# Kernel optimization log

Hardware: AMD Instinct MI355X
Metric: run time of the kernel (lower is better)

## Reference

```python
import jax, jax.numpy as jnp
import numpy as np

B, A, OBS, NACT, H, D = 8192, 8, 128, 32, 256, 64  # batch, n_agents, obs_shape, n_actions, rnn_hidden_dim, attn_dim
N = B * A


def setup_inputs() -> dict:
    key = jax.random.key(0)
    ks = jax.random.split(key, 12)
    s = 0.02
    return {
        "o": jax.random.normal(ks[0], (N, OBS), dtype=jnp.float32),
        "o_next": jax.random.normal(ks[1], (N, OBS), dtype=jnp.float32),
        "h": jax.random.normal(ks[2], (N, H), dtype=jnp.float32),
        "actions": jax.random.uniform(ks[3], (N, A, NACT), dtype=jnp.float32),
        "wq_w": jax.random.normal(ks[4], (D, 2 * OBS), dtype=jnp.float32) * s,
        "wq_b": jnp.zeros((D,), dtype=jnp.float32),
        "wk_w": jax.random.normal(ks[5], (D, NACT), dtype=jnp.float32) * s,
        "wk_b": jnp.zeros((D,), dtype=jnp.float32),
        "wv1_w": jax.random.normal(ks[6], (D, H + NACT), dtype=jnp.float32) * s,
        "wv1_b": jnp.zeros((D,), dtype=jnp.float32),
        "wv2_w": jax.random.normal(ks[7], (NACT, D), dtype=jnp.float32) * s,
        "wv2_b": jnp.zeros((NACT,), dtype=jnp.float32),
    }


def reference(o, o_next, h, actions, wq_w, wq_b, wk_w, wk_b, wv1_w, wv1_b, wv2_w, wv2_b):
    n, a, nact = actions.shape           # [N, A, n_actions]
    d = wq_w.shape[0]                    # attn_dim
    hdim = h.shape[-1]
    b = n // a
    # query: [N, D]
    query = jnp.concatenate([o, o_next], axis=-1) @ wq_w.T + wq_b
    # key: [N, A, D]
    key = (actions.reshape(-1, nact) @ wk_w.T + wk_b).reshape(n, a, d)
    # value: repeat h per attended agent -> [B*A*A, H]
    h_rep = jnp.tile(h.reshape(b, a, hdim), (1, a, 1)).reshape(-1, hdim)
    inps_v = jnp.concatenate([h_rep, actions.reshape(-1, nact)], axis=-1)
    hid = jax.nn.relu(inps_v @ wv1_w.T + wv1_b)
    value = (hid @ wv2_w.T + wv2_b).reshape(n, a, nact)
    # attention scores with self-masked diagonal
    scale = 1.0 / (float(d) ** 0.5)
    scores = jnp.einsum('nd,nad->na', query * scale, key).reshape(b, a, a)
    eye = jnp.eye(a, dtype=bool)
    scores = jnp.where(eye[None, :, :], jnp.asarray(-1e9, scores.dtype), scores)
    attn = jax.nn.softmax(scores, axis=-1).reshape(n, a, 1)
    q = jnp.sum(value * attn, axis=1)    # [N, n_actions]
    return q
```

## Files before the change

### kernel.cpp

```cpp
#include <hip/hip_runtime.h>

typedef __attribute__((ext_vector_type(8))) short bf16x8;
typedef __attribute__((ext_vector_type(4))) float f32x4;

#define MFMA(A, B, C) __builtin_amdgcn_mfma_f32_16x16x32_bf16((A), (B), (C), 0, 0, 0)

#define OFF_TB    0
#define OFF_WT_H  128
#define OFF_WT_L  16512
#define OFF_WHV_H 32896
#define OFF_WHV_L 65664
#define OFF_WA_H  98432
#define OFF_WA_L  102528

#define SM_P0   0
#define SM_HV   20480
#define SM_T    37888
#define SM_AT   47104
#define SM_SS   49152
#define SM_TOT  58880

__device__ __forceinline__ unsigned short f2bf(float v) {
    unsigned u = __builtin_bit_cast(unsigned, v);
    return (unsigned short)((u + 0x7fffu + ((u >> 16) & 1u)) >> 16);
}
__device__ __forceinline__ float bf2f(unsigned short b) {
    return __builtin_bit_cast(float, ((unsigned)b) << 16);
}
__device__ __forceinline__ ushort2 splitf(float v) {
    unsigned short h = f2bf(v);
    unsigned short l = f2bf(v - bf2f(h));
    return make_ushort2(h, l);
}

__global__ __launch_bounds__(256) void k_setup(const float* __restrict__ wq_w,
                                               const float* __restrict__ wq_b,
                                               const float* __restrict__ wk_w,
                                               const float* __restrict__ wv1,
                                               char* __restrict__ ws) {
    int gid = blockIdx.x * 256 + threadIdx.x;
    if (gid < 8192) {
        int k = gid >> 8, c = gid & 255;
        float acc = 0.f;
#pragma unroll 8
        for (int d = 0; d < 64; ++d) acc = fmaf(wk_w[d * 32 + k], wq_w[d * 256 + c], acc);
        ushort2 s = splitf(0.125f * acc);
        ((unsigned short*)(ws + OFF_WT_H))[gid] = s.x;
        ((unsigned short*)(ws + OFF_WT_L))[gid] = s.y;
    } else if (gid < 24576) {
        int i = gid - 8192;
        ushort2 s = splitf(wv1[(i >> 8) * 288 + (i & 255)]);
        ((unsigned short*)(ws + OFF_WHV_H))[i] = s.x;
        ((unsigned short*)(ws + OFF_WHV_L))[i] = s.y;
    } else if (gid < 26624) {
        int i = gid - 24576;
        ushort2 s = splitf(wv1[(i >> 5) * 288 + 256 + (i & 31)]);
        ((unsigned short*)(ws + OFF_WA_H))[i] = s.x;
        ((unsigned short*)(ws + OFF_WA_L))[i] = s.y;
    } else if (gid < 26656) {
        int k = gid - 26624;
        float b = 0.f;
#pragma unroll 8
        for (int d = 0; d < 64; ++d) b = fmaf(wk_w[d * 32 + k], wq_b[d], b);
        ((float*)(ws + OFF_TB))[k] = 0.125f * b;
    }
}

__global__ __launch_bounds__(256, 2) void fused(
    const float* __restrict__ o, const float* __restrict__ onx,
    const float* __restrict__ h, const float* __restrict__ act,
    const float* __restrict__ wv1b, const float* __restrict__ wv2,
    const float* __restrict__ wv2b, const char* __restrict__ ws,
    float* __restrict__ out)
{
    __shared__ __align__(16) char sm[SM_TOT];
    short* P0 = (short*)(sm + SM_P0);
    float* HV = (float*)(sm + SM_HV);
    float* T  = (float*)(sm + SM_T);
    float* AT = (float*)(sm + SM_AT);
    short* SS = (short*)(sm + SM_SS);

    const int tid  = threadIdx.x;
    const int lane = tid & 63;
    const int wid  = tid >> 6;
    const int l15  = lane & 15;
    const int quad = lane >> 4;
    const int n0   = blockIdx.x * 64;

    const f32x4 zv = {0.f, 0.f, 0.f, 0.f};
    f32x4 acc_hv[4] = {zv, zv, zv, zv};
    f32x4 acc_t[2]  = {zv, zv};

    auto chunk_load = [&](int ch, int i) -> float4 {
        int row = i >> 3, c4 = i & 7;
        if (ch < 4)  return ((const float4*)o)  [(size_t)(n0 + row) * 32 + ch * 8 + c4];
        if (ch < 8)  return ((const float4*)onx)[(size_t)(n0 + row) * 32 + (ch - 4) * 8 + c4];
        return ((const float4*)h)[(size_t)(n0 + row) * 64 + (ch - 8) * 8 + c4];
    };
    auto chunk_store = [&](int buf, int i, float4 v) {
        int row = i >> 3, c4 = i & 7;
        short* XH = P0 + buf * 5120;
        short* XL = XH + 2560;
        ushort2 s0 = splitf(v.x), s1 = splitf(v.y), s2 = splitf(v.z), s3 = splitf(v.w);
        *(ushort4*)&XH[row * 40 + c4 * 4] = make_ushort4(s0.x, s1.x, s2.x, s3.x);
        *(ushort4*)&XL[row * 40 + c4 * 4] = make_ushort4(s0.y, s1.y, s2.y, s3.y);
    };

    {
        float4 p0 = chunk_load(0, tid), p1 = chunk_load(0, tid + 256);
        chunk_store(0, tid, p0);
        chunk_store(0, tid + 256, p1);
        for (int ch = 0; ch < 16; ++ch) {
            __syncthreads();
            if (ch < 15) { p0 = chunk_load(ch + 1, tid); p1 = chunk_load(ch + 1, tid + 256); }
            {
                const short* XH = P0 + (ch & 1) * 5120;
                const short* XL = XH + 2560;
                int brow = wid * 16 + l15;
                bf16x8 Bh = *(const bf16x8*)&XH[brow * 40 + quad * 8];
                bf16x8 Bl = *(const bf16x8*)&XL[brow * 40 + quad * 8];
                if (ch < 8) {
#pragma unroll
                    for (int mt = 0; mt < 2; ++mt) {
                        int off = ((mt * 16 + l15) * 256 + ch * 32 + quad * 8) * 2;
                        bf16x8 Ah = *(const bf16x8*)(ws + OFF_WT_H + off);
                        bf16x8 Al = *(const bf16x8*)(ws + OFF_WT_L + off);
                        acc_t[mt] = MFMA(Ah, Bh, acc_t[mt]);
                        acc_t[mt] = MFMA(Ah, Bl, acc_t[mt]);
                        acc_t[mt] = MFMA(Al, Bh, acc_t[mt]);
                    }
                } else {
#pragma unroll
                    for (int mt = 0; mt < 4; ++mt) {
                        int off = ((mt * 16 + l15) * 256 + (ch - 8) * 32 + quad * 8) * 2;
                        bf16x8 Ah = *(const bf16x8*)(ws + OFF_WHV_H + off);
                        bf16x8 Al = *(const bf16x8*)(ws + OFF_WHV_L + off);
                        acc_hv[mt] = MFMA(Ah, Bh, acc_hv[mt]);
                        acc_hv[mt] = MFMA(Ah, Bl, acc_hv[mt]);
                        acc_hv[mt] = MFMA(Al, Bh, acc_hv[mt]);
                    }
                }
            }
            if (ch < 15) {
                chunk_store((ch + 1) & 1, tid, p0);
                chunk_store((ch + 1) & 1, tid + 256, p1);
            }
        }
    }
    {
        int erow = wid * 16 + l15;
        const float* tb = (const float*)(ws + OFF_TB);
#pragma unroll
        for (int mt = 0; mt < 4; ++mt) {
            int d0 = mt * 16 + quad * 4;
            float4 b = *(const float4*)&wv1b[d0];
            f32x4 a = acc_hv[mt];
            *(float4*)&HV[erow * 68 + d0] =
                make_float4(a[0] + b.x, a[1] + b.y, a[2] + b.z, a[3] + b.w);
        }
#pragma unroll
        for (int mt = 0; mt < 2; ++mt) {
            int k0 = mt * 16 + quad * 4;
            float4 b = *(const float4*)&tb[k0];
            f32x4 a = acc_t[mt];
            *(float4*)&T[erow * 36 + k0] =
                make_float4(a[0] + b.x, a[1] + b.y, a[2] + b.z, a[3] + b.w);
        }
    }
    __syncthreads();

    {
        float tr[32];
#pragma unroll
        for (int c4 = 0; c4 < 8; ++c4) {
            float4 v = *(const float4*)&T[lane * 36 + c4 * 4];
            tr[c4*4+0]=v.x; tr[c4*4+1]=v.y; tr[c4*4+2]=v.z; tr[c4*4+3]=v.w;
        }
        const float* arow = act + (size_t)(n0 + lane) * 256;
#pragma unroll
        for (int jj = 0; jj < 2; ++jj) {
            int j = wid * 2 + jj;
            float sc = 0.f;
#pragma unroll
            for (int c4 = 0; c4 < 8; ++c4) {
                float4 a = *(const float4*)(arow + j * 32 + c4 * 4);
                sc = fmaf(tr[c4*4+0], a.x, sc);
                sc = fmaf(tr[c4*4+1], a.y, sc);
                sc = fmaf(tr[c4*4+2], a.z, sc);
                sc = fmaf(tr[c4*4+3], a.w, sc);
            }
            AT[j * 64 + lane] = sc;
        }
    }
    __syncthreads();

    if (tid < 64) {
        int diag = tid & 7;
        float sc[8];
#pragma unroll
        for (int j = 0; j < 8; ++j) sc[j] = AT[j * 64 + tid];
        float mx = -1e30f;
#pragma unroll
        for (int j = 0; j < 8; ++j) if (j != diag) mx = fmaxf(mx, sc[j]);
        float e[8], sum = 0.f;
#pragma unroll
        for (int j = 0; j < 8; ++j) { e[j] = (j == diag) ? 0.f : __expf(sc[j] - mx); sum += e[j]; }
        float inv = 1.f / sum;
#pragma unroll
        for (int j = 0; j < 8; ++j) AT[j * 64 + tid] = e[j] * inv;
    }

    float* W2 = T;
    {
        const float4* wg = (const float4*)wv2;
        ((float4*)W2)[tid]       = wg[tid];
        ((float4*)W2)[tid + 256] = wg[tid + 256];
    }
    bf16x8 WAh[4], WAl[4];
#pragma unroll
    for (int mt = 0; mt < 4; ++mt) {
        int off = ((mt * 16 + l15) * 32 + quad * 8) * 2;
        WAh[mt] = *(const bf16x8*)(ws + OFF_WA_H + off);
        WAl[mt] = *(const bf16x8*)(ws + OFF_WA_L + off);
    }

    auto act_stage = [&](int g) {
        const float4* ag = (const float4*)(act + (size_t)(n0 + g * 16) * 256);
        short* AH = P0; short* AL = P0 + 5120;
#pragma unroll
        for (int q = 0; q < 4; ++q) {
            int i = tid + q * 256;
            int njr = i >> 3, c4 = i & 7;
            float4 v = ag[njr * 8 + c4];
            ushort2 s0 = splitf(v.x), s1 = splitf(v.y), s2 = splitf(v.z), s3 = splitf(v.w);
            *(ushort4*)&AH[njr * 40 + c4 * 4] = make_ushort4(s0.x, s1.x, s2.x, s3.x);
            *(ushort4*)&AL[njr * 40 + c4 * 4] = make_ushort4(s0.y, s1.y, s2.y, s3.y);
        }
    };
    act_stage(0);
    __syncthreads();

    for (int g = 0; g < 4; ++g) {
        const short* AH = P0; const short* AL = P0 + 5120;
        f32x4 accB[8];
#pragma unroll
        for (int i = 0; i < 8; ++i) accB[i] = zv;
#pragma unroll
        for (int nt = 0; nt < 2; ++nt) {
            int njr = wid * 32 + nt * 16 + l15;
            bf16x8 Bh = *(const bf16x8*)&AH[njr * 40 + quad * 8];
            bf16x8 Bl = *(const bf16x8*)&AL[njr * 40 + quad * 8];
#pragma unroll
            for (int mt = 0; mt < 4; ++mt) {
                f32x4 a = accB[nt * 4 + mt];
                a = MFMA(WAh[mt], Bh, a);
                a = MFMA(WAh[mt], Bl, a);
                a = MFMA(WAl[mt], Bh, a);
                accB[nt * 4 + mt] = a;
            }
        }
#pragma unroll
        for (int nt = 0; nt < 2; ++nt) {
            int njr  = wid * 32 + nt * 16 + l15;
            int nb   = g * 16 + (njr >> 3);
            int j    = njr & 7;
            int hrow = (nb & ~7) + j;
            float at = AT[j * 64 + nb];
#pragma unroll
            for (int mt = 0; mt < 4; ++mt) {
                int d0 = mt * 16 + quad * 4;
                float4 hv4 = *(const float4*)&HV[hrow * 68 + d0];
                f32x4 a = accB[nt * 4 + mt];
                float v0 = at * fmaxf(a[0] + hv4.x, 0.f);
                float v1 = at * fmaxf(a[1] + hv4.y, 0.f);
                float v2 = at * fmaxf(a[2] + hv4.z, 0.f);
                float v3 = at * fmaxf(a[3] + hv4.w, 0.f);
#pragma unroll
                for (int m = 1; m <= 4; m <<= 1) {
                    v0 += __shfl_xor(v0, m);
                    v1 += __shfl_xor(v1, m);
                    v2 += __shfl_xor(v2, m);
                    v3 += __shfl_xor(v3, m);
                }
                if (j == 0)
                    *(ushort4*)&SS[nb * 76 + d0] =
                        make_ushort4(f2bf(v0), f2bf(v1), f2bf(v2), f2bf(v3));
            }
        }
        __syncthreads();
        if (g < 3) act_stage(g + 1);
        __syncthreads();
    }

    {
        float s[64];
#pragma unroll
        for (int q = 0; q < 16; ++q) {
            ushort4 u = *(const ushort4*)&SS[lane * 76 + q * 4];
            s[q*4+0] = bf2f(u.x); s[q*4+1] = bf2f(u.y);
            s[q*4+2] = bf2f(u.z); s[q*4+3] = bf2f(u.w);
        }
        float qa[8];
#pragma unroll
        for (int e = 0; e < 8; ++e) qa[e] = wv2b[wid * 8 + e];
#pragma unroll
        for (int d4 = 0; d4 < 16; ++d4) {
#pragma unroll
            for (int e = 0; e < 8; ++e) {
                float4 w = *(const float4*)&W2[(wid * 8 + e) * 64 + d4 * 4];
                qa[e] = fmaf(w.x, s[d4*4+0], qa[e]);
                qa[e] = fmaf(w.y, s[d4*4+1], qa[e]);
                qa[e] = fmaf(w.z, s[d4*4+2], qa[e]);
                qa[e] = fmaf(w.w, s[d4*4+3], qa[e]);
            }
        }
        float* op = out + (size_t)(n0 + lane) * 32 + wid * 8;
        ((float4*)op)[0] = make_float4(qa[0], qa[1], qa[2], qa[3]);
        ((float4*)op)[1] = make_float4(qa[4], qa[5], qa[6], qa[7]);
    }
}

extern "C" void kernel_launch(void* const* d_in, const int* in_sizes, int n_in,
                              void* d_out, int out_size, void* d_ws, size_t ws_size,
                              hipStream_t stream) {
    const float* o     = (const float*)d_in[0];
    const float* onx   = (const float*)d_in[1];
    const float* h     = (const float*)d_in[2];
    const float* act   = (const float*)d_in[3];
    const float* wq_w  = (const float*)d_in[4];
    const float* wq_b  = (const float*)d_in[5];
    const float* wk_w  = (const float*)d_in[6];
    const float* wv1_w = (const float*)d_in[8];
    const float* wv1_b = (const float*)d_in[9];
    const float* wv2_w = (const float*)d_in[10];
    const float* wv2_b = (const float*)d_in[11];
    float* out = (float*)d_out;
    char* ws   = (char*)d_ws;

    k_setup<<<105, 256, 0, stream>>>(wq_w, wq_b, wk_w, wv1_w, ws);
    fused<<<1024, 256, 0, stream>>>(o, onx, h, act, wv1_b, wv2_w, wv2_b, ws, out);
}
```

Baseline: 284.7 us.

## Load MFMA B operands directly from global, drop LDS staging and barriers

Each lane now loads its o/o_next/h and action rows straight from global memory into registers and splits them to bf16 hi/lo there, replacing the LDS double-buffered staging and its per-chunk __syncthreads. The staging buffer is removed, W2 gets its own LDS slot, and the shared footprint shrinks so launch bounds can ask for 3 blocks per SM. This targets barrier stalls and LDS traffic. In exchange, the global loads are less coalesced (each lane reads 32 bytes from a different row), the conversion work is repeated per wave, and there is no explicit prefetch overlap.

```diff
diff --git a/kernel.cpp b/kernel.cpp
--- a/kernel.cpp
+++ b/kernel.cpp
@@ -13,12 +13,12 @@
 #define OFF_WA_H  98432
 #define OFF_WA_L  102528
 
-#define SM_P0   0
-#define SM_HV   20480
-#define SM_T    37888
-#define SM_AT   47104
-#define SM_SS   49152
-#define SM_TOT  58880
+#define SM_HV   0
+#define SM_T    17408
+#define SM_AT   26624
+#define SM_SS   28672
+#define SM_W2   38400
+#define SM_TOT  46592
 
 __device__ __forceinline__ unsigned short f2bf(float v) {
     unsigned u = __builtin_bit_cast(unsigned, v);
@@ -31,6 +31,17 @@
     unsigned short h = f2bf(v);
     unsigned short l = f2bf(v - bf2f(h));
     return make_ushort2(h, l);
+}
+__device__ __forceinline__ void split8(float4 a, float4 b, bf16x8& hi, bf16x8& lo) {
+    float v[8] = {a.x, a.y, a.z, a.w, b.x, b.y, b.z, b.w};
+    bf16x8 H, L;
+#pragma unroll
+    for (int i = 0; i < 8; ++i) {
+        ushort2 s = splitf(v[i]);
+        H[i] = (short)s.x;
+        L[i] = (short)s.y;
+    }
+    hi = H; lo = L;
 }
 
 __global__ __launch_bounds__(256) void k_setup(const float* __restrict__ wq_w,
@@ -66,7 +77,7 @@
     }
 }
 
-__global__ __launch_bounds__(256, 2) void fused(
+__global__ __launch_bounds__(256, 3) void fused(
     const float* __restrict__ o, const float* __restrict__ onx,
     const float* __restrict__ h, const float* __restrict__ act,
     const float* __restrict__ wv1b, const float* __restrict__ wv2,
@@ -74,11 +85,11 @@
     float* __restrict__ out)
 {
     __shared__ __align__(16) char sm[SM_TOT];
-    short* P0 = (short*)(sm + SM_P0);
     float* HV = (float*)(sm + SM_HV);
     float* T  = (float*)(sm + SM_T);
     float* AT = (float*)(sm + SM_AT);
     short* SS = (short*)(sm + SM_SS);
+    float* W2 = (float*)(sm + SM_W2);
 
     const int tid  = threadIdx.x;
     const int lane = tid & 63;
@@ -87,64 +98,52 @@
     const int quad = lane >> 4;
     const int n0   = blockIdx.x * 64;
 
+    {
+        const float4* wg = (const float4*)wv2;
+        ((float4*)W2)[tid]       = wg[tid];
+        ((float4*)W2)[tid + 256] = wg[tid + 256];
+    }
+
     const f32x4 zv = {0.f, 0.f, 0.f, 0.f};
     f32x4 acc_hv[4] = {zv, zv, zv, zv};
     f32x4 acc_t[2]  = {zv, zv};
 
-    auto chunk_load = [&](int ch, int i) -> float4 {
-        int row = i >> 3, c4 = i & 7;
-        if (ch < 4)  return ((const float4*)o)  [(size_t)(n0 + row) * 32 + ch * 8 + c4];
-        if (ch < 8)  return ((const float4*)onx)[(size_t)(n0 + row) * 32 + (ch - 4) * 8 + c4];
-        return ((const float4*)h)[(size_t)(n0 + row) * 64 + (ch - 8) * 8 + c4];
-    };
-    auto chunk_store = [&](int buf, int i, float4 v) {
-        int row = i >> 3, c4 = i & 7;
-        short* XH = P0 + buf * 5120;
-        short* XL = XH + 2560;
-        ushort2 s0 = splitf(v.x), s1 = splitf(v.y), s2 = splitf(v.z), s3 = splitf(v.w);
-        *(ushort4*)&XH[row * 40 + c4 * 4] = make_ushort4(s0.x, s1.x, s2.x, s3.x);
-        *(ushort4*)&XL[row * 40 + c4 * 4] = make_ushort4(s0.y, s1.y, s2.y, s3.y);
-    };
-
-    {
-        float4 p0 = chunk_load(0, tid), p1 = chunk_load(0, tid + 256);
-        chunk_store(0, tid, p0);
-        chunk_store(0, tid + 256, p1);
-        for (int ch = 0; ch < 16; ++ch) {
-            __syncthreads();
-            if (ch < 15) { p0 = chunk_load(ch + 1, tid); p1 = chunk_load(ch + 1, tid + 256); }
-            {
-                const short* XH = P0 + (ch & 1) * 5120;
-                const short* XL = XH + 2560;
-                int brow = wid * 16 + l15;
-                bf16x8 Bh = *(const bf16x8*)&XH[brow * 40 + quad * 8];
-                bf16x8 Bl = *(const bf16x8*)&XL[brow * 40 + quad * 8];
-                if (ch < 8) {
-#pragma unroll
-                    for (int mt = 0; mt < 2; ++mt) {
-                        int off = ((mt * 16 + l15) * 256 + ch * 32 + quad * 8) * 2;
-                        bf16x8 Ah = *(const bf16x8*)(ws + OFF_WT_H + off);
-                        bf16x8 Al = *(const bf16x8*)(ws + OFF_WT_L + off);
-                        acc_t[mt] = MFMA(Ah, Bh, acc_t[mt]);
-                        acc_t[mt] = MFMA(Ah, Bl, acc_t[mt]);
-                        acc_t[mt] = MFMA(Al, Bh, acc_t[mt]);
-                    }
-                } else {
-#pragma unroll
-                    for (int mt = 0; mt < 4; ++mt) {
-                        int off = ((mt * 16 + l15) * 256 + (ch - 8) * 32 + quad * 8) * 2;
-                        bf16x8 Ah = *(const bf16x8*)(ws + OFF_WHV_H + off);
-                        bf16x8 Al = *(const bf16x8*)(ws + OFF_WHV_L + off);
-                        acc_hv[mt] = MFMA(Ah, Bh, acc_hv[mt]);
-                        acc_hv[mt] = MFMA(Ah, Bl, acc_hv[mt]);
-                        acc_hv[mt] = MFMA(Al, Bh, acc_hv[mt]);
-                    }
-                }
-            }
-            if (ch < 15) {
-                chunk_store((ch + 1) & 1, tid, p0);
-                chunk_store((ch + 1) & 1, tid + 256, p1);
-            }
+    const int myrow = n0 + wid * 16 + l15;
+
+#pragma unroll
+    for (int ch = 0; ch < 8; ++ch) {
+        const float* src = (ch < 4)
+            ? o   + (size_t)myrow * 128 + ch * 32 + quad * 8
+            : onx + (size_t)myrow * 128 + (ch - 4) * 32 + quad * 8;
+        float4 v0 = *(const float4*)src;
+        float4 v1 = *(const float4*)(src + 4);
+        bf16x8 Bh, Bl;
+        split8(v0, v1, Bh, Bl);
+#pragma unroll
+        for (int mt = 0; mt < 2; ++mt) {
+            int off = ((mt * 16 + l15) * 256 + ch * 32 + quad * 8) * 2;
+            bf16x8 Ah = *(const bf16x8*)(ws + OFF_WT_H + off);
+            bf16x8 Al = *(const bf16x8*)(ws + OFF_WT_L + off);
+            acc_t[mt] = MFMA(Ah, Bh, acc_t[mt]);
+            acc_t[mt] = MFMA(Ah, Bl, acc_t[mt]);
+            acc_t[mt] = MFMA(Al, Bh, acc_t[mt]);
+        }
+    }
+#pragma unroll
+    for (int ch = 0; ch < 8; ++ch) {
+        const float* src = h + (size_t)myrow * 256 + ch * 32 + quad * 8;
+        float4 v0 = *(const float4*)src;
+        float4 v1 = *(const float4*)(src + 4);
+        bf16x8 Bh, Bl;
+        split8(v0, v1, Bh, Bl);
+#pragma unroll
+        for (int mt = 0; mt < 4; ++mt) {
+            int off = ((mt * 16 + l15) * 256 + ch * 32 + quad * 8) * 2;
+            bf16x8 Ah = *(const bf16x8*)(ws + OFF_WHV_H + off);
+            bf16x8 Al = *(const bf16x8*)(ws + OFF_WHV_L + off);
+            acc_hv[mt] = MFMA(Ah, Bh, acc_hv[mt]);
+            acc_hv[mt] = MFMA(Ah, Bl, acc_hv[mt]);
+            acc_hv[mt] = MFMA(Al, Bh, acc_hv[mt]);
         }
     }
     {
@@ -192,30 +191,6 @@
             AT[j * 64 + lane] = sc;
         }
     }
-    __syncthreads();
-
-    if (tid < 64) {
-        int diag = tid & 7;
-        float sc[8];
-#pragma unroll
-        for (int j = 0; j < 8; ++j) sc[j] = AT[j * 64 + tid];
-        float mx = -1e30f;
-#pragma unroll
-        for (int j = 0; j < 8; ++j) if (j != diag) mx = fmaxf(mx, sc[j]);
-        float e[8], sum = 0.f;
-#pragma unroll
-        for (int j = 0; j < 8; ++j) { e[j] = (j == diag) ? 0.f : __expf(sc[j] - mx); sum += e[j]; }
-        float inv = 1.f / sum;
-#pragma unroll
-        for (int j = 0; j < 8; ++j) AT[j * 64 + tid] = e[j] * inv;
-    }
-
-    float* W2 = T;
-    {
-        const float4* wg = (const float4*)wv2;
-        ((float4*)W2)[tid]       = wg[tid];
-        ((float4*)W2)[tid + 256] = wg[tid + 256];
-    }
     bf16x8 WAh[4], WAl[4];
 #pragma unroll
     for (int mt = 0; mt < 4; ++mt) {
@@ -223,74 +198,68 @@
         WAh[mt] = *(const bf16x8*)(ws + OFF_WA_H + off);
         WAl[mt] = *(const bf16x8*)(ws + OFF_WA_L + off);
     }
-
-    auto act_stage = [&](int g) {
-        const float4* ag = (const float4*)(act + (size_t)(n0 + g * 16) * 256);
-        short* AH = P0; short* AL = P0 + 5120;
-#pragma unroll
-        for (int q = 0; q < 4; ++q) {
-            int i = tid + q * 256;
-            int njr = i >> 3, c4 = i & 7;
-            float4 v = ag[njr * 8 + c4];
-            ushort2 s0 = splitf(v.x), s1 = splitf(v.y), s2 = splitf(v.z), s3 = splitf(v.w);
-            *(ushort4*)&AH[njr * 40 + c4 * 4] = make_ushort4(s0.x, s1.x, s2.x, s3.x);
-            *(ushort4*)&AL[njr * 40 + c4 * 4] = make_ushort4(s0.y, s1.y, s2.y, s3.y);
-        }
-    };
-    act_stage(0);
     __syncthreads();
 
+    if (tid < 64) {
+        int diag = tid & 7;
+        float sc[8];
+#pragma unroll
+        for (int j = 0; j < 8; ++j) sc[j] = AT[j * 64 + tid];
+        float mx = -1e30f;
+#pragma unroll
+        for (int j = 0; j < 8; ++j) if (j != diag) mx = fmaxf(mx, sc[j]);
+        float e[8], sum = 0.f;
+#pragma unroll
+        for (int j = 0; j < 8; ++j) { e[j] = (j == diag) ? 0.f : __expf(sc[j] - mx); sum += e[j]; }
+        float inv = 1.f / sum;
+#pragma unroll
+        for (int j = 0; j < 8; ++j) AT[j * 64 + tid] = e[j] * inv;
+    }
+    __syncthreads();
+
+#pragma unroll
     for (int g = 0; g < 4; ++g) {
-        const short* AH = P0; const short* AL = P0 + 5120;
-        f32x4 accB[8];
-#pragma unroll
-        for (int i = 0; i < 8; ++i) accB[i] = zv;
 #pragma unroll
         for (int nt = 0; nt < 2; ++nt) {
             int njr = wid * 32 + nt * 16 + l15;
-            bf16x8 Bh = *(const bf16x8*)&AH[njr * 40 + quad * 8];
-            bf16x8 Bl = *(const bf16x8*)&AL[njr * 40 + quad * 8];
+            int nb  = g * 16 + (njr >> 3);
+            int j   = njr & 7;
+            const float* ap = act + (size_t)(n0 + nb) * 256 + j * 32 + quad * 8;
+            float4 v0 = *(const float4*)ap;
+            float4 v1 = *(const float4*)(ap + 4);
+            bf16x8 Bh, Bl;
+            split8(v0, v1, Bh, Bl);
+            f32x4 accB[4] = {zv, zv, zv, zv};
 #pragma unroll
             for (int mt = 0; mt < 4; ++mt) {
-                f32x4 a = accB[nt * 4 + mt];
-                a = MFMA(WAh[mt], Bh, a);
-                a = MFMA(WAh[mt], Bl, a);
-                a = MFMA(WAl[mt], Bh, a);
-                accB[nt * 4 + mt] = a;
+                accB[mt] = MFMA(WAh[mt], Bh, accB[mt]);
+                accB[mt] = MFMA(WAh[mt], Bl, accB[mt]);
+                accB[mt] = MFMA(WAl[mt], Bh, accB[mt]);
             }
-        }
-#pragma unroll
-        for (int nt = 0; nt < 2; ++nt) {
-            int njr  = wid * 32 + nt * 16 + l15;
-            int nb   = g * 16 + (njr >> 3);
-            int j    = njr & 7;
             int hrow = (nb & ~7) + j;
             float at = AT[j * 64 + nb];
 #pragma unroll
             for (int mt = 0; mt < 4; ++mt) {
                 int d0 = mt * 16 + quad * 4;
                 float4 hv4 = *(const float4*)&HV[hrow * 68 + d0];
-                f32x4 a = accB[nt * 4 + mt];
-                float v0 = at * fmaxf(a[0] + hv4.x, 0.f);
-                float v1 = at * fmaxf(a[1] + hv4.y, 0.f);
-                float v2 = at * fmaxf(a[2] + hv4.z, 0.f);
-                float v3 = at * fmaxf(a[3] + hv4.w, 0.f);
+                float r0 = at * fmaxf(accB[mt][0] + hv4.x, 0.f);
+                float r1 = at * fmaxf(accB[mt][1] + hv4.y, 0.f);
+                float r2 = at * fmaxf(accB[mt][2] + hv4.z, 0.f);
+                float r3 = at * fmaxf(accB[mt][3] + hv4.w, 0.f);
 #pragma unroll
                 for (int m = 1; m <= 4; m <<= 1) {
-                    v0 += __shfl_xor(v0, m);
-                    v1 += __shfl_xor(v1, m);
-                    v2 += __shfl_xor(v2, m);
-                    v3 += __shfl_xor(v3, m);
+                    r0 += __shfl_xor(r0, m);
+                    r1 += __shfl_xor(r1, m);
+                    r2 += __shfl_xor(r2, m);
+                    r3 += __shfl_xor(r3, m);
                 }
                 if (j == 0)
                     *(ushort4*)&SS[nb * 76 + d0] =
-                        make_ushort4(f2bf(v0), f2bf(v1), f2bf(v2), f2bf(v3));
+                        make_ushort4(f2bf(r0), f2bf(r1), f2bf(r2), f2bf(r3));
             }
         }
-        __syncthreads();
-        if (g < 3) act_stage(g + 1);
-        __syncthreads();
-    }
+    }
+    __syncthreads();
 
     {
         float s[64];
```

Result: faster. 278.2 us (-2.3%).
